# Optimization experiments

Measured on AMD Instinct MI355X. Metric: run time of the kernel, lower is better.

Reference implementation:

```python
import jax, jax.numpy as jnp
import numpy as np

MASK_THR = 0.005   # cfg.mask_thr
SIGMA = 2.0        # cfg.sigma (gaussian kernel)
N, G, H, W = 500, 128, 200, 304


def setup_inputs() -> dict:
    key = jax.random.key(0)
    k1, k2, k3, k4, k5, k6 = jax.random.split(key, 6)
    return {
        "cate_scores": jax.random.uniform(k1, (N,), jnp.float32),
        "seg_preds_x": jax.random.uniform(k2, (G, H, W), jnp.float32),
        "seg_preds_y": jax.random.uniform(k3, (G, H, W), jnp.float32),
        "cate_labels": jax.random.randint(k4, (N,), 0, 80),
        "x_inds": jax.random.randint(k5, (N,), 0, G),
        "y_inds": jax.random.randint(k6, (N,), 0, G),
    }


def reference(cate_scores, seg_preds_x, seg_preds_y, cate_labels, x_inds, y_inds):
    # --- SOLO decoupled mask decoding: irregular grid-index gather ---
    mask_x = seg_preds_x[x_inds]                 # [N,H,W]
    mask_y = seg_preds_y[y_inds]                 # [N,H,W]
    soft = mask_x * mask_y                       # seg_masks_soft
    hard = (soft > MASK_THR).astype(soft.dtype)  # seg_masks (binary)
    sum_masks = hard.sum((1, 2))                 # [N] mask areas
    # mask-quality rescoring
    seg_score = (soft * hard).sum((1, 2)) / jnp.maximum(sum_masks, 1.0)
    scores = cate_scores * seg_score

    # --- Matrix NMS (gaussian kernel) ---
    flat = hard.reshape(N, -1)                   # [N, H*W]
    inter = flat @ flat.T                        # [N,N] intersection areas
    union = sum_masks[:, None] + sum_masks[None, :] - inter
    iou = jnp.triu(inter / jnp.maximum(union, 1e-6), k=1)
    label_eq = jnp.triu((cate_labels[:, None] == cate_labels[None, :]).astype(soft.dtype), k=1)
    decay_iou = iou * label_eq                   # same-class IoU, upper tri
    comp_iou = decay_iou.max(0)                  # [N] max IoU with higher-scored same-class mask
    decay_matrix = jnp.exp(-SIGMA * decay_iou ** 2)
    comp_matrix = jnp.exp(-SIGMA * comp_iou ** 2)[:, None]  # expand(n,n).T in torch
    decay_coef = (decay_matrix / comp_matrix).min(0)         # [N]
    return scores * decay_coef
```

## Files before the change

kernel.cpp:

```cpp
#include <hip/hip_runtime.h>


#define N_DET 500
#define HW    (200 * 304)
#define TILE  64
#define NT    (HW / TILE)
#define PSTR  512
#define DSTR  950
#define NW2   (NT / 2)
#define MASK_THR 0.005f
#define SIGMA 2.0f

__global__ __launch_bounds__(512) void maskgen_kernel(
    const float* __restrict__ seg_x, const float* __restrict__ seg_y,
    const int* __restrict__ x_inds, const int* __restrict__ y_inds,
    unsigned long long* __restrict__ packed_t,
    float* __restrict__ part_sum)
{
    __shared__ __align__(16) float sx[128 * 64];
    __shared__ __align__(16) float sy[128 * 64];
    const int t   = blockIdx.x;
    const int tid = threadIdx.x;
    const int base = t * TILE;

    for (int e = tid; e < 128 * 16; e += 512) {
        const int r  = e >> 4;
        const int c4 = (e & 15) << 2;
        *(float4*)(sx + (r << 6) + c4) = *(const float4*)(seg_x + (size_t)r * HW + base + c4);
        *(float4*)(sy + (r << 6) + c4) = *(const float4*)(seg_y + (size_t)r * HW + base + c4);
    }
    __syncthreads();

    if (tid < N_DET) {
        const float4* __restrict__ rx4 = (const float4*)(sx + (x_inds[tid] << 6));
        const float4* __restrict__ ry4 = (const float4*)(sy + (y_inds[tid] << 6));
        float ssum = 0.0f;
        unsigned long long w = 0ull;
        #pragma unroll
        for (int k = 0; k < 16; ++k) {
            const int f = (k + tid) & 15;
            const float4 xv = rx4[f];
            const float4 yv = ry4[f];
            const float p0 = xv.x * yv.x, p1 = xv.y * yv.y,
                        p2 = xv.z * yv.z, p3 = xv.w * yv.w;
            const int b0 = p0 > MASK_THR, b1 = p1 > MASK_THR,
                      b2 = p2 > MASK_THR, b3 = p3 > MASK_THR;
            ssum += (b0 ? p0 : 0.0f) + (b1 ? p1 : 0.0f)
                  + (b2 ? p2 : 0.0f) + (b3 ? p3 : 0.0f);
            const unsigned int nib = (unsigned)(b0 | (b1 << 1) | (b2 << 2) | (b3 << 3));
            w |= (unsigned long long)nib << (f << 2);
        }
        packed_t[(size_t)t * PSTR + tid] = w;
        part_sum[(size_t)t * PSTR + tid] = ssum;
    }
}

__global__ __launch_bounds__(512) void transpose_kernel(
    const unsigned long long* __restrict__ packed_t,
    const float* __restrict__ part_sum,
    unsigned long long* __restrict__ packed_d,
    float* __restrict__ part_sumT)
{
    __shared__ unsigned long long tp[64 * 65];
    __shared__ float              ts[64 * 65];
    const int t0  = blockIdx.x * 64;
    const int d0  = blockIdx.y * 64;
    const int tid = threadIdx.x;
    const int lane = tid & 63, wav = tid >> 6;

    #pragma unroll
    for (int k = 0; k < 8; ++k) {
        const int r  = (k << 3) + wav;
        const int gt = t0 + r;
        unsigned long long v = 0ull; float s = 0.0f;
        if (gt < NT) {
            v = packed_t[(size_t)gt * PSTR + d0 + lane];
            s = part_sum[(size_t)gt * PSTR + d0 + lane];
        }
        tp[r * 65 + lane] = v;
        ts[r * 65 + lane] = s;
    }
    __syncthreads();
    const int gt = t0 + lane;
    #pragma unroll
    for (int k = 0; k < 8; ++k) {
        const int m = (k << 3) + wav;
        const int d = d0 + m;
        if (gt < NT && d < N_DET) {
            packed_d [(size_t)d * DSTR + gt] = tp[lane * 65 + m];
            part_sumT[(size_t)d * DSTR + gt] = ts[lane * 65 + m];
        }
    }
}

__global__ __launch_bounds__(256) void pair_iou_kernel(
    const unsigned long long* __restrict__ packed_d,
    const float* __restrict__ part_sumT,
    const int* __restrict__ labels,
    const float* __restrict__ cate_scores,
    float* __restrict__ d2col,
    float* __restrict__ comp2,
    float* __restrict__ scores)
{
    const int j   = blockIdx.x;
    const int tid = threadIdx.x;
    const int lane = tid & 63, wav = tid >> 6;

    __shared__ int   s_lab[N_DET];
    __shared__ int   s_list[N_DET];
    __shared__ int   s_cnt;
    __shared__ float s_red[4];
    __shared__ float s_max[4];

    if (tid == 0) s_cnt = 0;
    for (int i = tid; i < N_DET; i += 256) {
        s_lab[i] = labels[i];
        d2col[(size_t)j * N_DET + i] = 0.0f;
    }
    __syncthreads();

    const int lj = s_lab[j];
    for (int i = tid; i < j; i += 256)
        if (s_lab[i] == lj) { const int p = atomicAdd(&s_cnt, 1); s_list[p] = i; }

    const ulonglong2* __restrict__ pj2 = (const ulonglong2*)(packed_d + (size_t)j * DSTR);
    ulonglong2 bj[8];
    float cj_part = 0.0f;
    #pragma unroll
    for (int q = 0; q < 8; ++q) {
        const int w = lane + (q << 6);
        if (w < NW2) {
            bj[q] = pj2[w];
            cj_part += (float)(__popcll(bj[q].x) + __popcll(bj[q].y));
        } else { bj[q].x = 0ull; bj[q].y = 0ull; }
    }
    #pragma unroll
    for (int off = 32; off; off >>= 1) cj_part += __shfl_down(cj_part, off);
    const float cj = __shfl(cj_part, 0);

    float S = 0.0f;
    for (int t = tid; t < NT; t += 256) S += part_sumT[(size_t)j * DSTR + t];
    #pragma unroll
    for (int off = 32; off; off >>= 1) S += __shfl_down(S, off);
    if (lane == 0) s_red[wav] = S;
    __syncthreads();
    if (tid == 0) {
        const float Sj = s_red[0] + s_red[1] + s_red[2] + s_red[3];
        scores[j] = cate_scores[j] * (Sj / fmaxf(cj, 1.0f));
    }
    const int cnt = s_cnt;

    float wmax = 0.0f;
    for (int p = wav; p < cnt; p += 4) {
        const int i = s_list[p];
        const ulonglong2* __restrict__ pi2 = (const ulonglong2*)(packed_d + (size_t)i * DSTR);
        int inter = 0, ci = 0;
        #pragma unroll
        for (int q = 0; q < 8; ++q) {
            const int w = lane + (q << 6);
            if (w < NW2) {
                const ulonglong2 a = pi2[w];
                inter += __popcll(a.x & bj[q].x) + __popcll(a.y & bj[q].y);
                ci    += __popcll(a.x) + __popcll(a.y);
            }
        }
        #pragma unroll
        for (int off = 32; off; off >>= 1) {
            inter += __shfl_down(inter, off);
            ci    += __shfl_down(ci,    off);
        }
        if (lane == 0) {
            const float uni = (float)ci + cj - (float)inter;
            const float iou = (float)inter / fmaxf(uni, 1e-6f);
            d2col[(size_t)j * N_DET + i] = iou * iou;
            wmax = fmaxf(wmax, iou);
        }
    }
    if (lane == 0) s_max[wav] = wmax;
    __syncthreads();
    if (tid == 0) {
        const float c = fmaxf(fmaxf(s_max[0], s_max[1]), fmaxf(s_max[2], s_max[3]));
        comp2[j] = c * c;
    }
}

__global__ __launch_bounds__(64) void decay_kernel(
    const float* __restrict__ d2col,
    const float* __restrict__ comp2,
    const float* __restrict__ scores,
    float* __restrict__ out)
{
    const int j = blockIdx.x;
    const int lane = threadIdx.x;
    float m = 1e30f;
    for (int i = lane; i < N_DET; i += 64)
        m = fminf(m, comp2[i] - d2col[(size_t)j * N_DET + i]);
    #pragma unroll
    for (int off = 32; off; off >>= 1)
        m = fminf(m, __shfl_down(m, off));
    if (lane == 0) out[j] = scores[j] * expf(SIGMA * m);
}

extern "C" void kernel_launch(void* const* d_in, const int* in_sizes, int n_in,
                              void* d_out, int out_size, void* d_ws, size_t ws_size,
                              hipStream_t stream) {
    const float* cate_scores = (const float*)d_in[0];
    const float* seg_x       = (const float*)d_in[1];
    const float* seg_y       = (const float*)d_in[2];
    const int*   labels      = (const int*)d_in[3];
    const int*   x_inds      = (const int*)d_in[4];
    const int*   y_inds      = (const int*)d_in[5];
    float* out = (float*)d_out;

    char* ws = (char*)d_ws;
    unsigned long long* packed_t = (unsigned long long*)(ws + 0);
    float* part_sum  = (float*)(ws + 3891200);
    unsigned long long* packed_d = (unsigned long long*)(ws + 5836800);
    float* part_sumT = (float*)(ws + 9636800);
    float* d2col     = (float*)(ws + 11536800);
    float* scores    = (float*)(ws + 12536800);
    float* comp2     = (float*)(ws + 12538800);

    maskgen_kernel  <<<NT, 512, 0, stream>>>(seg_x, seg_y, x_inds, y_inds,
                                             packed_t, part_sum);
    transpose_kernel<<<dim3(15, 8), 512, 0, stream>>>(packed_t, part_sum,
                                                      packed_d, part_sumT);
    pair_iou_kernel <<<N_DET, 256, 0, stream>>>(packed_d, part_sumT, labels,
                                                cate_scores, d2col, comp2, scores);
    decay_kernel    <<<N_DET, 64, 0, stream>>>(d2col, comp2, scores, out);
}
```

Before: 125.3 us.

## Reduce mask sums and counts in transpose; store sparse same-class IoU lists

The transpose kernel now reduces per-detection soft sums and popcounts and accumulates them atomically. This removes the transposed partial-sum array and the per-pair popcount of mask i. Pair IoU writes only the same-class pairs into a compact per-column list, replacing the dense zero-filled d2col matrix. The decay kernel takes the min over comp2 for all entries and only the listed pairs, and also computes the rescored score. The change adds a memset and atomics, and the float atomic accumulation order is nondeterministic.

```diff
diff --git a/kernel.cpp b/kernel.cpp
--- a/kernel.cpp
+++ b/kernel.cpp
@@ -8,6 +8,7 @@
 #define PSTR  512
 #define DSTR  950
 #define NW2   (NT / 2)
+#define CAP   512
 #define MASK_THR 0.005f
 #define SIGMA 2.0f
 
@@ -59,7 +60,8 @@
     const unsigned long long* __restrict__ packed_t,
     const float* __restrict__ part_sum,
     unsigned long long* __restrict__ packed_d,
-    float* __restrict__ part_sumT)
+    float* __restrict__ ssum_acc,
+    int*   __restrict__ cnt_acc)
 {
     __shared__ unsigned long long tp[64 * 65];
     __shared__ float              ts[64 * 65];
@@ -81,98 +83,99 @@
         ts[r * 65 + lane] = s;
     }
     __syncthreads();
+
     const int gt = t0 + lane;
     #pragma unroll
     for (int k = 0; k < 8; ++k) {
         const int m = (k << 3) + wav;
         const int d = d0 + m;
-        if (gt < NT && d < N_DET) {
-            packed_d [(size_t)d * DSTR + gt] = tp[lane * 65 + m];
-            part_sumT[(size_t)d * DSTR + gt] = ts[lane * 65 + m];
-        }
+        if (gt < NT && d < N_DET)
+            packed_d[(size_t)d * DSTR + gt] = tp[lane * 65 + m];
+    }
+
+    const int dl = tid >> 3;
+    const int q  = tid & 7;
+    float S = 0.0f; int C = 0;
+    #pragma unroll
+    for (int k = 0; k < 8; ++k) {
+        const int r = (k << 3) + q;
+        S += ts[r * 65 + dl];
+        C += __popcll(tp[r * 65 + dl]);
+    }
+    #pragma unroll
+    for (int d = 4; d; d >>= 1) {
+        S += __shfl_down(S, d, 8);
+        C += __shfl_down(C, d, 8);
+    }
+    const int dg = d0 + dl;
+    if (q == 0 && dg < N_DET) {
+        atomicAdd(ssum_acc + dg, S);
+        atomicAdd(cnt_acc + dg, C);
     }
 }
 
 __global__ __launch_bounds__(256) void pair_iou_kernel(
     const unsigned long long* __restrict__ packed_d,
-    const float* __restrict__ part_sumT,
     const int* __restrict__ labels,
-    const float* __restrict__ cate_scores,
-    float* __restrict__ d2col,
+    const int* __restrict__ cnt_acc,
     float* __restrict__ comp2,
-    float* __restrict__ scores)
+    float* __restrict__ pd2,
+    int*   __restrict__ pidx,
+    int*   __restrict__ pcnt)
 {
     const int j   = blockIdx.x;
     const int tid = threadIdx.x;
     const int lane = tid & 63, wav = tid >> 6;
 
     __shared__ int   s_lab[N_DET];
+    __shared__ float s_cf[N_DET];
     __shared__ int   s_list[N_DET];
     __shared__ int   s_cnt;
-    __shared__ float s_red[4];
     __shared__ float s_max[4];
 
     if (tid == 0) s_cnt = 0;
     for (int i = tid; i < N_DET; i += 256) {
         s_lab[i] = labels[i];
-        d2col[(size_t)j * N_DET + i] = 0.0f;
-    }
-    __syncthreads();
-
-    const int lj = s_lab[j];
+        s_cf[i]  = (float)cnt_acc[i];
+    }
+    __syncthreads();
+
+    const int   lj = s_lab[j];
+    const float cj = s_cf[j];
     for (int i = tid; i < j; i += 256)
         if (s_lab[i] == lj) { const int p = atomicAdd(&s_cnt, 1); s_list[p] = i; }
+    __syncthreads();
+    const int cnt = s_cnt;
 
     const ulonglong2* __restrict__ pj2 = (const ulonglong2*)(packed_d + (size_t)j * DSTR);
     ulonglong2 bj[8];
-    float cj_part = 0.0f;
     #pragma unroll
     for (int q = 0; q < 8; ++q) {
         const int w = lane + (q << 6);
-        if (w < NW2) {
-            bj[q] = pj2[w];
-            cj_part += (float)(__popcll(bj[q].x) + __popcll(bj[q].y));
-        } else { bj[q].x = 0ull; bj[q].y = 0ull; }
-    }
-    #pragma unroll
-    for (int off = 32; off; off >>= 1) cj_part += __shfl_down(cj_part, off);
-    const float cj = __shfl(cj_part, 0);
-
-    float S = 0.0f;
-    for (int t = tid; t < NT; t += 256) S += part_sumT[(size_t)j * DSTR + t];
-    #pragma unroll
-    for (int off = 32; off; off >>= 1) S += __shfl_down(S, off);
-    if (lane == 0) s_red[wav] = S;
-    __syncthreads();
-    if (tid == 0) {
-        const float Sj = s_red[0] + s_red[1] + s_red[2] + s_red[3];
-        scores[j] = cate_scores[j] * (Sj / fmaxf(cj, 1.0f));
-    }
-    const int cnt = s_cnt;
+        if (w < NW2) bj[q] = pj2[w];
+        else { bj[q].x = 0ull; bj[q].y = 0ull; }
+    }
 
     float wmax = 0.0f;
     for (int p = wav; p < cnt; p += 4) {
         const int i = s_list[p];
         const ulonglong2* __restrict__ pi2 = (const ulonglong2*)(packed_d + (size_t)i * DSTR);
-        int inter = 0, ci = 0;
+        int inter = 0;
         #pragma unroll
         for (int q = 0; q < 8; ++q) {
             const int w = lane + (q << 6);
             if (w < NW2) {
                 const ulonglong2 a = pi2[w];
                 inter += __popcll(a.x & bj[q].x) + __popcll(a.y & bj[q].y);
-                ci    += __popcll(a.x) + __popcll(a.y);
             }
         }
         #pragma unroll
-        for (int off = 32; off; off >>= 1) {
-            inter += __shfl_down(inter, off);
-            ci    += __shfl_down(ci,    off);
-        }
+        for (int off = 32; off; off >>= 1) inter += __shfl_down(inter, off);
         if (lane == 0) {
-            const float uni = (float)ci + cj - (float)inter;
+            const float uni = s_cf[i] + cj - (float)inter;
             const float iou = (float)inter / fmaxf(uni, 1e-6f);
-            d2col[(size_t)j * N_DET + i] = iou * iou;
+            pd2 [(size_t)j * CAP + p] = iou * iou;
+            pidx[(size_t)j * CAP + p] = i;
             wmax = fmaxf(wmax, iou);
         }
     }
@@ -181,24 +184,35 @@
     if (tid == 0) {
         const float c = fmaxf(fmaxf(s_max[0], s_max[1]), fmaxf(s_max[2], s_max[3]));
         comp2[j] = c * c;
+        pcnt[j]  = cnt;
     }
 }
 
 __global__ __launch_bounds__(64) void decay_kernel(
-    const float* __restrict__ d2col,
     const float* __restrict__ comp2,
-    const float* __restrict__ scores,
+    const float* __restrict__ pd2,
+    const int*   __restrict__ pidx,
+    const int*   __restrict__ pcnt,
+    const float* __restrict__ ssum_acc,
+    const int*   __restrict__ cnt_acc,
+    const float* __restrict__ cate_scores,
     float* __restrict__ out)
 {
     const int j = blockIdx.x;
     const int lane = threadIdx.x;
     float m = 1e30f;
-    for (int i = lane; i < N_DET; i += 64)
-        m = fminf(m, comp2[i] - d2col[(size_t)j * N_DET + i]);
+    for (int i = lane; i < N_DET; i += 64) m = fminf(m, comp2[i]);
+    const int c = pcnt[j];
+    for (int k = lane; k < c; k += 64)
+        m = fminf(m, comp2[pidx[(size_t)j * CAP + k]] - pd2[(size_t)j * CAP + k]);
     #pragma unroll
     for (int off = 32; off; off >>= 1)
         m = fminf(m, __shfl_down(m, off));
-    if (lane == 0) out[j] = scores[j] * expf(SIGMA * m);
+    if (lane == 0) {
+        const float C = (float)cnt_acc[j];
+        const float score = cate_scores[j] * (ssum_acc[j] / fmaxf(C, 1.0f));
+        out[j] = score * expf(SIGMA * m);
+    }
 }
 
 extern "C" void kernel_launch(void* const* d_in, const int* in_sizes, int n_in,
@@ -214,18 +228,22 @@
 
     char* ws = (char*)d_ws;
     unsigned long long* packed_t = (unsigned long long*)(ws + 0);
-    float* part_sum  = (float*)(ws + 3891200);
-    unsigned long long* packed_d = (unsigned long long*)(ws + 5836800);
-    float* part_sumT = (float*)(ws + 9636800);
-    float* d2col     = (float*)(ws + 11536800);
-    float* scores    = (float*)(ws + 12536800);
-    float* comp2     = (float*)(ws + 12538800);
-
+    unsigned long long* packed_d = (unsigned long long*)(ws + 3891200);
+    float* pd2      = (float*)(ws + 7691200);
+    int*   pidx     = (int*)  (ws + 8715200);
+    int*   pcnt     = (int*)  (ws + 9739200);
+    float* comp2    = (float*)(ws + 9741200);
+    float* ssum_acc = (float*)(ws + 9743200);
+    int*   cnt_acc  = (int*)  (ws + 9745200);
+    float* part_sum = (float*)(ws + 9747200);
+
+    hipMemsetAsync(ws + 9743200, 0, 4000, stream);
     maskgen_kernel  <<<NT, 512, 0, stream>>>(seg_x, seg_y, x_inds, y_inds,
                                              packed_t, part_sum);
     transpose_kernel<<<dim3(15, 8), 512, 0, stream>>>(packed_t, part_sum,
-                                                      packed_d, part_sumT);
-    pair_iou_kernel <<<N_DET, 256, 0, stream>>>(packed_d, part_sumT, labels,
-                                                cate_scores, d2col, comp2, scores);
-    decay_kernel    <<<N_DET, 64, 0, stream>>>(d2col, comp2, scores, out);
-}
+                                                      packed_d, ssum_acc, cnt_acc);
+    pair_iou_kernel <<<N_DET, 256, 0, stream>>>(packed_d, labels, cnt_acc,
+                                                comp2, pd2, pidx, pcnt);
+    decay_kernel    <<<N_DET, 64, 0, stream>>>(comp2, pd2, pidx, pcnt,
+                                               ssum_acc, cnt_acc, cate_scores, out);
+}
```

After: 125.9 us. Within noise of the previous version (+0.5%).
